# Kernel optimization log

Measured on AMD Instinct MI355X. Metric: run time of the kernel, lower is better.

The kernel has to match this reference:

```python
import jax, jax.numpy as jnp
import numpy as np

B, S, H = 32, 256, 1024   # batch, seq_len, xlmr hidden
HL = 512                  # lstm hidden per direction
E = 256                   # entity_feature_size
L = 5                     # languages: en fr de es it
LN_EPS = 1e-5


def setup_inputs() -> dict:
    key = jax.random.key(0)
    ks = jax.random.split(key, 12)
    sc = 0.02
    sequence_output = jax.random.normal(ks[0], (B, S, H), jnp.float32)
    lengths = jax.random.randint(ks[1], (B,), S // 2, S + 1)
    attention_mask = (jnp.arange(S)[None, :] < lengths[:, None]).astype(jnp.int32)
    language_ids = jax.random.randint(ks[2], (B,), 0, L).astype(jnp.int64)
    # per-language adapter params (stacked over lang dim)
    W1 = jax.random.normal(ks[3], (L, H, H), jnp.float32) * sc
    b1 = jnp.zeros((L, H), jnp.float32)
    ln_g = jnp.ones((L, H), jnp.float32)
    ln_b = jnp.zeros((L, H), jnp.float32)
    W2 = jax.random.normal(ks[4], (L, H, H), jnp.float32) * sc
    b2 = jnp.zeros((L, H), jnp.float32)
    # BiLSTM params, torch gate order (i, f, g, o); b = b_ih + b_hh
    Wih_f = jax.random.normal(ks[5], (4 * HL, H), jnp.float32) * sc
    Whh_f = jax.random.normal(ks[6], (4 * HL, HL), jnp.float32) * sc
    b_f = jnp.zeros((4 * HL,), jnp.float32)
    Wih_b = jax.random.normal(ks[7], (4 * HL, H), jnp.float32) * sc
    Whh_b = jax.random.normal(ks[8], (4 * HL, HL), jnp.float32) * sc
    b_b = jnp.zeros((4 * HL,), jnp.float32)
    # projection 2*HL -> E
    Wp = jax.random.normal(ks[9], (E, 2 * HL), jnp.float32) * sc
    bp = jnp.zeros((E,), jnp.float32)
    return dict(sequence_output=sequence_output, attention_mask=attention_mask,
                language_ids=language_ids, W1=W1, b1=b1, ln_g=ln_g, ln_b=ln_b,
                W2=W2, b2=b2, Wih_f=Wih_f, Whh_f=Whh_f, b_f=b_f,
                Wih_b=Wih_b, Whh_b=Whh_b, b_b=b_b, Wp=Wp, bp=bp)


def _lstm_scan(x, mask, Wih, Whh, b):
    """x: [S,B,H], mask: [S,B,1] bool. Returns hidden states [S,B,HL].
    Masked steps keep state and emit 0 (pack/pad_packed semantics)."""
    h0 = jnp.zeros((x.shape[1], Whh.shape[1]), x.dtype)

    def step(carry, inp):
        h, c = carry
        x_t, m = inp
        gates = x_t @ Wih.T + h @ Whh.T + b
        i, f, g, o = jnp.split(gates, 4, axis=-1)
        c_new = jax.nn.sigmoid(f) * c + jax.nn.sigmoid(i) * jnp.tanh(g)
        h_new = jax.nn.sigmoid(o) * jnp.tanh(c_new)
        h = jnp.where(m, h_new, h)
        c = jnp.where(m, c_new, c)
        return (h, c), jnp.where(m, h_new, 0.0)

    _, ys = jax.lax.scan(step, (h0, h0), (x, mask))
    return ys


def reference(sequence_output, attention_mask, language_ids, W1, b1, ln_g, ln_b,
              W2, b2, Wih_f, Whh_f, b_f, Wih_b, Whh_b, b_b, Wp, bp):
    # --- all 5 language adapters on the full batch, then masked-sum ---
    h = jnp.einsum('bsh,lhd->lbsd', sequence_output, W1) + b1[:, None, None, :]
    mu = h.mean(-1, keepdims=True)
    var = h.var(-1, keepdims=True)
    h = (h - mu) * jax.lax.rsqrt(var + LN_EPS) * ln_g[:, None, None, :] + ln_b[:, None, None, :]
    h = jax.nn.relu(h)
    h = jnp.einsum('lbsd,ldh->lbsh', h, W2) + b2[:, None, None, :]
    onehot = jax.nn.one_hot(language_ids, L, dtype=h.dtype)          # [B,L]
    adapted = jnp.einsum('lbsh,bl->bsh', h, onehot)                  # [B,S,H]
    # --- BiLSTM over valid lengths (packed-sequence semantics) ---
    x = adapted.transpose(1, 0, 2)                                    # [S,B,H]
    m = attention_mask.astype(bool).T[:, :, None]                     # [S,B,1]
    ys_f = _lstm_scan(x, m, Wih_f, Whh_f, b_f)                        # [S,B,HL]
    ys_b = _lstm_scan(x[::-1], m[::-1], Wih_b, Whh_b, b_b)[::-1]      # [S,B,HL]
    lstm_out = jnp.concatenate([ys_f, ys_b], -1).transpose(1, 0, 2)   # [B,S,2HL]
    return lstm_out @ Wp.T + bp                                       # [B,S,E]
```

## Files before the change

kernel.cpp:

```cpp
#include <hip/hip_runtime.h>

typedef __bf16 bft;
typedef bft bf16x8 __attribute__((ext_vector_type(8)));
typedef bft bf16x4 __attribute__((ext_vector_type(4)));
typedef bft bf16x2 __attribute__((ext_vector_type(2)));
typedef float f32x4 __attribute__((ext_vector_type(4)));
typedef unsigned long long u64;
typedef unsigned int u32;
typedef u32 u32x4 __attribute__((ext_vector_type(4)));

#define LN_EPS 1e-5f
#define SENT 0x7FC17FC1u


__device__ __forceinline__ float sigmoidf_(float x) {
    return 1.f / (1.f + __expf(-x));
}
__device__ __forceinline__ float tanhf_(float x) {
    float e = __expf(-2.f * fabsf(x));
    float t = (1.f - e) / (1.f + e);
    return copysignf(t, x);
}

__global__ void cvt_f32_bf16(const float* __restrict__ in, bft* __restrict__ out, int n4) {
    int i = blockIdx.x * blockDim.x + threadIdx.x;
    if (i < n4) {
        float4 v = ((const float4*)in)[i];
        bf16x4 o = { (bft)v.x, (bft)v.y, (bft)v.z, (bft)v.w };
        ((bf16x4*)out)[i] = o;
    }
}

__global__ void init_hg(u32* __restrict__ hg) {
    int i = blockIdx.x * blockDim.x + threadIdx.x;
    int buf = (i >> 13) & 3;
    hg[i] = (buf == 0) ? 0u : SENT;
}

__global__ void pack_mask(const int* __restrict__ mask, u32* __restrict__ mbits) {
    int t = blockIdx.x * blockDim.x + threadIdx.x;
    if (t < 256) {
        int w = t >> 5, b = t & 31;
        u32 v = 0;
        for (int i = 0; i < 32; ++i)
            v |= (mask[b * 256 + w * 32 + i] ? 1u : 0u) << i;
        mbits[w * 32 + b] = v;
    }
}

__global__ __launch_bounds__(256) void cvt_permute_wih(
    const float* __restrict__ in, bft* __restrict__ out)
{
    int r = blockIdx.x;
    int src = (r & 3) * 512 + (r >> 2);
    int t = threadIdx.x;
    float4 v = ((const float4*)(in + (size_t)src * 1024))[t];
    bf16x4 o = { (bft)v.x, (bft)v.y, (bft)v.z, (bft)v.w };
    ((bf16x4*)(out + (size_t)r * 1024))[t] = o;
}

__global__ void permute_bias(const float* __restrict__ in, float* __restrict__ out) {
    int t = blockIdx.x * blockDim.x + threadIdx.x;
    if (t < 2048) out[t] = in[(t & 3) * 512 + (t >> 2)];
}

__global__ __launch_bounds__(256) void transpose_cvt_w(
    const float* __restrict__ W1, const float* __restrict__ W2,
    bft* __restrict__ W1t, bft* __restrict__ W2t)
{
    __shared__ float tile[32][33];
    int z = blockIdx.z;
    int l = z >> 1;
    const float* src = ((z & 1) ? W2 : W1) + ((size_t)l << 20);
    bft* dst = ((z & 1) ? W2t : W1t) + ((size_t)l << 20);
    int tx = threadIdx.x & 31, ty = threadIdx.x >> 5;
    int bx = blockIdx.x * 32, by = blockIdx.y * 32;
    for (int r = ty; r < 32; r += 8)
        tile[r][tx] = src[(size_t)(by + r) * 1024 + bx + tx];
    __syncthreads();
    for (int r = ty; r < 32; r += 8)
        dst[(size_t)(bx + r) * 1024 + by + tx] = (bft)tile[tx][r];
}

__global__ __launch_bounds__(256) void gemm_bt(
    const bft* __restrict__ A, const bft* __restrict__ Bt,
    const float* __restrict__ bias, const int* __restrict__ langs,
    int langStrideB, int langStrideBias,
    float* __restrict__ outF, bft* __restrict__ outB,
    int remapLog, int remapMul, int ldc)
{
    const int K = 1024;
    int tn = blockIdx.x, tm = blockIdx.y;
    int row0 = tm * 128, col0 = tn * 128;
    int lang = langs ? langs[row0 >> 8] : 0;
    const bft* Ap = A + (size_t)row0 * K;
    const bft* Bp = Bt + (size_t)lang * langStrideB + (size_t)col0 * K;
    const float* biasp = bias + (size_t)lang * langStrideBias + col0;

    __shared__ bft As[128 * 32];
    __shared__ bft Bs[128 * 32];

    int t = threadIdx.x;
    int lane = t & 63, wave = t >> 6;
    int wm = wave & 1, wn = wave >> 1;
    int lrow = lane & 15, quad = lane >> 4;

    f32x4 acc[4][4] = {};

    for (int k0 = 0; k0 < K; k0 += 32) {
        __syncthreads();
        for (int c = t; c < 512; c += 256) {
            int r = c >> 2, co = (c & 3) << 3;
            *(uint4*)(As + r * 32 + co) = *(const uint4*)(Ap + (size_t)r * K + k0 + co);
            *(uint4*)(Bs + r * 32 + co) = *(const uint4*)(Bp + (size_t)r * K + k0 + co);
        }
        __syncthreads();
        bf16x8 af[4], bfr[4];
#pragma unroll
        for (int i = 0; i < 4; ++i)
            af[i] = *(const bf16x8*)(As + (wm * 64 + i * 16 + lrow) * 32 + quad * 8);
#pragma unroll
        for (int j = 0; j < 4; ++j)
            bfr[j] = *(const bf16x8*)(Bs + (wn * 64 + j * 16 + lrow) * 32 + quad * 8);
#pragma unroll
        for (int i = 0; i < 4; ++i)
#pragma unroll
            for (int j = 0; j < 4; ++j)
                acc[i][j] = __builtin_amdgcn_mfma_f32_16x16x32_bf16(af[i], bfr[j], acc[i][j], 0, 0, 0);
    }

#pragma unroll
    for (int i = 0; i < 4; ++i) {
#pragma unroll
        for (int j = 0; j < 4; ++j) {
#pragma unroll
            for (int r = 0; r < 4; ++r) {
                int m = wm * 64 + i * 16 + quad * 4 + r;
                int n = wn * 64 + j * 16 + lrow;
                int grow = row0 + m;
                float v = acc[i][j][r] + biasp[n];
                size_t idx;
                if (remapLog < 0) {
                    int b = grow >> 8, s = grow & 255;
                    int col = col0 + n;
                    int jj = col >> 2, gg = col & 3;
                    int jp = jj & 7, gs = jj >> 3;
                    int tc = (((b >> 4) * 2 + (jp >> 2)) << 6) + ((jp & 3) << 4) + (b & 15);
                    idx = (((size_t)s * 64 + gs) << 10) + (tc << 2) + gg;
                } else {
                    int orow = remapLog ? ((grow & ((1 << remapLog) - 1)) * remapMul + (grow >> remapLog))
                                        : grow;
                    idx = (size_t)orow * ldc + col0 + n;
                }
                if (outF) outF[idx] = v;
                else outB[idx] = (bft)v;
            }
        }
    }
}

__global__ __launch_bounds__(256) void ln_relu_kernel(
    const float* __restrict__ h1, bft* __restrict__ a2,
    const float* __restrict__ ln_g, const float* __restrict__ ln_b,
    const int* __restrict__ langs)
{
    int row = blockIdx.x;
    int lang = langs[row >> 8];
    const float* x = h1 + (size_t)row * 1024;
    int t = threadIdx.x;
    float4 v = ((const float4*)x)[t];
    float s = v.x + v.y + v.z + v.w;
    float ss = v.x * v.x + v.y * v.y + v.z * v.z + v.w * v.w;
#pragma unroll
    for (int off = 32; off > 0; off >>= 1) {
        s += __shfl_down(s, off, 64);
        ss += __shfl_down(ss, off, 64);
    }
    __shared__ float red[8];
    int wave = t >> 6, lane = t & 63;
    if (lane == 0) { red[wave] = s; red[4 + wave] = ss; }
    __syncthreads();
    float S = red[0] + red[1] + red[2] + red[3];
    float SS = red[4] + red[5] + red[6] + red[7];
    float mean = S * (1.f / 1024.f);
    float var = SS * (1.f / 1024.f) - mean * mean;
    float inv = rsqrtf(var + LN_EPS);
    float4 g = ((const float4*)(ln_g + (size_t)lang * 1024))[t];
    float4 b = ((const float4*)(ln_b + (size_t)lang * 1024))[t];
    float y0 = fmaxf(0.f, (v.x - mean) * inv * g.x + b.x);
    float y1 = fmaxf(0.f, (v.y - mean) * inv * g.y + b.y);
    float y2 = fmaxf(0.f, (v.z - mean) * inv * g.z + b.z);
    float y3 = fmaxf(0.f, (v.w - mean) * inv * g.w + b.w);
    bf16x4 o = { (bft)y0, (bft)y1, (bft)y2, (bft)y3 };
    ((bf16x4*)(a2 + (size_t)row * 1024))[t] = o;
}

__global__ __launch_bounds__(256) void bilstm_kernel(
    const bft* __restrict__ gin_f, const bft* __restrict__ gin_b,
    const bft* __restrict__ Whh_f, const bft* __restrict__ Whh_b,
    const u32* __restrict__ mbits, bft* __restrict__ ys,
    u32* __restrict__ hg)
{
    __shared__ u64 smem[4096];
    bft* hs  = (bft*)smem;
    u32* hsd = (u32*)smem;

    int blk = blockIdx.x;
    int dir = blk >> 6;
    int gslice = blk & 63;
    const bft* Whh = dir ? Whh_b : Whh_f;
    const bft* gin = dir ? gin_b : gin_f;
    u32* hbase = hg + (size_t)dir * 4 * 8192;

    int t = threadIdx.x;
    int lane = t & 63, wave = t >> 6;
    int wm = wave & 1, wn = wave >> 1;
    int lrow = lane & 15, quad = lane >> 4;

    bf16x8 wf[16];
    {
        int row32 = wm * 16 + lrow;
        int jl = row32 >> 2, g = row32 & 3;
        const bft* wp = Whh + (size_t)(g * 512 + (gslice << 3) + jl) * 512 + quad * 8;
#pragma unroll
        for (int kk = 0; kk < 16; ++kk)
            wf[kk] = *(const bf16x8*)(wp + kk * 32);
    }

    int batch = wn * 16 + lrow;
    u32* ysU = (u32*)ys;
    float cs = 0.f, hp = 0.f;
    u32 mw = 0;

    for (int it = 0; it < 256; ++it) {
        int tt = dir ? (255 - it) : it;

        bf16x4 gv = *(const bf16x4*)(gin + ((((size_t)tt * 64 + gslice) << 10) + (t << 2)));
        if ((it & 31) == 0) mw = mbits[(tt >> 5) * 32 + batch];
        int mk = (mw >> (tt & 31)) & 1;

        if (!(lane & 16)) {
            u32* ca = hbase + (size_t)((it + 2) & 3) * 8192
                            + gslice * 128 + batch * 4 + wm * 2 + (quad >> 1);
            u32 sv = SENT;
            asm volatile("global_store_dword %0, %1, off sc0 sc1" :: "v"(ca), "v"(sv) : "memory");
        }

        __syncthreads();

        const u32* hq = hbase + (size_t)(it & 3) * 8192;
        u32x4 r[8];
        u32 need = 0xffu;
        for (;;) {
#pragma unroll
            for (int i = 0; i < 8; ++i)
                if (need & (1u << i))
                    asm volatile("global_load_dwordx4 %0, %1, off sc0 sc1"
                                 : "=v"(r[i]) : "v"(hq + i * 1024 + t * 4) : "memory");
            asm volatile("s_waitcnt vmcnt(0)" ::: "memory");
#pragma unroll
            for (int i = 0; i < 8; ++i)
                if ((need & (1u << i)) &&
                    r[i][0] != SENT && r[i][1] != SENT && r[i][2] != SENT && r[i][3] != SENT)
                    need &= ~(1u << i);
            if (!need) break;
            __builtin_amdgcn_s_sleep(2);
        }

#pragma unroll
        for (int i = 0; i < 8; ++i) {
            int bat = t & 31, gs = i * 8 + (t >> 5);
            *(u32x4*)(hsd + bat * 256 + ((gs ^ (bat & 7)) << 2)) = r[i];
        }
        __syncthreads();

        f32x4 acc0 = {}, acc1 = {};
#pragma unroll
        for (int kk = 0; kk < 16; ++kk) {
            int b16 = kk * 4 + quad;
            bf16x8 b = *(const bf16x8*)(hs + batch * 512 + ((b16 ^ (batch & 7)) << 3));
            if (kk & 1) acc1 = __builtin_amdgcn_mfma_f32_16x16x32_bf16(wf[kk], b, acc1, 0, 0, 0);
            else        acc0 = __builtin_amdgcn_mfma_f32_16x16x32_bf16(wf[kk], b, acc0, 0, 0, 0);
        }
        f32x4 acc = acc0 + acc1;

        float xi = acc[0] + (float)gv[0];
        float xf = acc[1] + (float)gv[1];
        float xg = acc[2] + (float)gv[2];
        float xo = acc[3] + (float)gv[3];
        float cn = sigmoidf_(xf) * cs + sigmoidf_(xi) * tanhf_(xg);
        float hn = sigmoidf_(xo) * tanhf_(cn);
        if (mk) { cs = cn; hp = hn; }
        union { bft h; unsigned short u; } hc; hc.h = (bft)hp;
        u32 own = (u32)hc.u | ((mk ? (u32)hc.u : 0u) << 16);
        u32 par = __shfl_xor(own, 16, 64);
        u32 hpair = (own & 0xffffu) | (par << 16);
        u32 ypair = (own >> 16) | (par & 0xffff0000u);

        if (!(lane & 16)) {
            u32* ha = hbase + (size_t)((it + 1) & 3) * 8192
                            + gslice * 128 + batch * 4 + wm * 2 + (quad >> 1);
            asm volatile("global_store_dword %0, %1, off sc0 sc1" :: "v"(ha), "v"(hpair) : "memory");
            ysU[((size_t)tt * 32 + batch) * 512 + dir * 256
                + (gslice << 2) + wm * 2 + (quad >> 1)] = ypair;
        }
    }
}

extern "C" void kernel_launch(void* const* d_in, const int* in_sizes, int n_in,
                              void* d_out, int out_size, void* d_ws, size_t ws_size,
                              hipStream_t stream)
{
    const float* X     = (const float*)d_in[0];
    const int*   amask = (const int*)d_in[1];
    const int*   langs = (const int*)d_in[2];
    const float* W1    = (const float*)d_in[3];
    const float* b1    = (const float*)d_in[4];
    const float* ln_g  = (const float*)d_in[5];
    const float* ln_b  = (const float*)d_in[6];
    const float* W2    = (const float*)d_in[7];
    const float* b2    = (const float*)d_in[8];
    const float* Wih_f = (const float*)d_in[9];
    const float* Whh_f = (const float*)d_in[10];
    const float* b_f   = (const float*)d_in[11];
    const float* Wih_b = (const float*)d_in[12];
    const float* Whh_b = (const float*)d_in[13];
    const float* b_b   = (const float*)d_in[14];
    const float* Wp    = (const float*)d_in[15];
    const float* bp    = (const float*)d_in[16];
    float* out = (float*)d_out;

    char* ws = (char*)d_ws;
    size_t off = 0;
    auto alloc = [&](size_t bytes) -> void* {
        void* p = ws + off;
        off += (bytes + 255) & ~(size_t)255;
        return p;
    };
    bft* Xbf   = (bft*)alloc(8192ull * 1024 * 2);
    bft* W1t   = (bft*)alloc(5ull * 1024 * 1024 * 2);
    bft* W2t   = (bft*)alloc(5ull * 1024 * 1024 * 2);
    bft* Wihf  = (bft*)alloc(2048ull * 1024 * 2);
    bft* Wihb  = (bft*)alloc(2048ull * 1024 * 2);
    bft* Whhf  = (bft*)alloc(2048ull * 512 * 2);
    bft* Whhb  = (bft*)alloc(2048ull * 512 * 2);
    bft* Wpb   = (bft*)alloc(256ull * 1024 * 2);
    float* h1  = (float*)alloc(8192ull * 1024 * 4);
    bft* a2    = (bft*)alloc(8192ull * 1024 * 2);
    bft* adapt = (bft*)alloc(8192ull * 1024 * 2);
    bft* ginf  = (bft*)alloc(256ull * 32 * 2048 * 2);
    bft* ginb  = (bft*)alloc(256ull * 32 * 2048 * 2);
    bft* ysb   = (bft*)alloc(256ull * 32 * 1024 * 2);
    float* pbf = (float*)alloc(2048ull * 4);
    float* pbb = (float*)alloc(2048ull * 4);
    u32* hg    = (u32*)alloc(2ull * 4 * 8192 * 4);
    u32* mbits = (u32*)alloc(256ull * 4);
    (void)ws_size; (void)in_sizes; (void)n_in; (void)out_size;

    auto cvt = [&](const float* src, bft* dst, int n) {
        int n4 = n >> 2;
        hipLaunchKernelGGL(cvt_f32_bf16, dim3((n4 + 255) / 256), dim3(256), 0, stream, src, dst, n4);
    };
    cvt(X, Xbf, 8192 * 1024);
    hipLaunchKernelGGL(cvt_permute_wih, dim3(2048), dim3(256), 0, stream, Wih_f, Wihf);
    hipLaunchKernelGGL(cvt_permute_wih, dim3(2048), dim3(256), 0, stream, Wih_b, Wihb);
    cvt(Whh_f, Whhf, 2048 * 512);
    cvt(Whh_b, Whhb, 2048 * 512);
    cvt(Wp, Wpb, 256 * 1024);
    hipLaunchKernelGGL(permute_bias, dim3(8), dim3(256), 0, stream, b_f, pbf);
    hipLaunchKernelGGL(permute_bias, dim3(8), dim3(256), 0, stream, b_b, pbb);
    hipLaunchKernelGGL(init_hg, dim3(256), dim3(256), 0, stream, hg);
    hipLaunchKernelGGL(pack_mask, dim3(1), dim3(256), 0, stream, amask, mbits);
    hipLaunchKernelGGL(transpose_cvt_w, dim3(32, 32, 10), dim3(256), 0, stream, W1, W2, W1t, W2t);

    hipLaunchKernelGGL(gemm_bt, dim3(8, 64), dim3(256), 0, stream,
        Xbf, W1t, b1, langs, 1024 * 1024, 1024, h1, (bft*)nullptr, 0, 0, 1024);
    hipLaunchKernelGGL(ln_relu_kernel, dim3(8192), dim3(256), 0, stream, h1, a2, ln_g, ln_b, langs);
    hipLaunchKernelGGL(gemm_bt, dim3(8, 64), dim3(256), 0, stream,
        a2, W2t, b2, langs, 1024 * 1024, 1024, (float*)nullptr, adapt, 0, 0, 1024);
    hipLaunchKernelGGL(gemm_bt, dim3(16, 64), dim3(256), 0, stream,
        adapt, Wihf, pbf, (const int*)nullptr, 0, 0, (float*)nullptr, ginf, -1, 0, 0);
    hipLaunchKernelGGL(gemm_bt, dim3(16, 64), dim3(256), 0, stream,
        adapt, Wihb, pbb, (const int*)nullptr, 0, 0, (float*)nullptr, ginb, -1, 0, 0);
    {
        void* args[] = { (void*)&ginf, (void*)&ginb, (void*)&Whhf, (void*)&Whhb,
                         (void*)&mbits, (void*)&ysb, (void*)&hg };
        hipLaunchCooperativeKernel((const void*)bilstm_kernel, dim3(128), dim3(256), args, 0, stream);
    }
    hipLaunchKernelGGL(gemm_bt, dim3(2, 64), dim3(256), 0, stream,
        ysb, Wpb, bp, (const int*)nullptr, 0, 0, out, (bft*)nullptr, 5, 256, 256);
}
```

Before: 1.276 ms.

## Load LSTM hidden state directly into MFMA registers and use global_load_lds in GEMM

The BiLSTM recurrence now lays out the global hidden-state exchange buffer batch-major, so each lane loads its MFMA B-operand fragments straight from global memory. This removes the LDS staging and both per-step __syncthreads, and each wave polls for the sentinel independently with a ballot. Block-to-direction mapping is interleaved so both directions spread across the device. The GEMM tile loads switch to global_load_lds to skip the register round trip. In exchange each lane issues twice as many global loads per poll, and the GEMM drops the explicit row/col tile layout, which relies on the linear LDS layout matching.

```diff
diff --git a/kernel.cpp b/kernel.cpp
--- a/kernel.cpp
+++ b/kernel.cpp
@@ -109,10 +109,16 @@
 
     for (int k0 = 0; k0 < K; k0 += 32) {
         __syncthreads();
-        for (int c = t; c < 512; c += 256) {
+#pragma unroll
+        for (int c0 = 0; c0 < 512; c0 += 256) {
+            int c = c0 + t;
             int r = c >> 2, co = (c & 3) << 3;
-            *(uint4*)(As + r * 32 + co) = *(const uint4*)(Ap + (size_t)r * K + k0 + co);
-            *(uint4*)(Bs + r * 32 + co) = *(const uint4*)(Bp + (size_t)r * K + k0 + co);
+            __builtin_amdgcn_global_load_lds(
+                (const __attribute__((address_space(1))) u32*)(Ap + (size_t)r * K + k0 + co),
+                (__attribute__((address_space(3))) u32*)(As + c * 8), 16, 0, 0);
+            __builtin_amdgcn_global_load_lds(
+                (const __attribute__((address_space(1))) u32*)(Bp + (size_t)r * K + k0 + co),
+                (__attribute__((address_space(3))) u32*)(Bs + c * 8), 16, 0, 0);
         }
         __syncthreads();
         bf16x8 af[4], bfr[4];
@@ -201,13 +207,9 @@
     const u32* __restrict__ mbits, bft* __restrict__ ys,
     u32* __restrict__ hg)
 {
-    __shared__ u64 smem[4096];
-    bft* hs  = (bft*)smem;
-    u32* hsd = (u32*)smem;
-
     int blk = blockIdx.x;
-    int dir = blk >> 6;
-    int gslice = blk & 63;
+    int dir = (blk & 7) >> 2;
+    int gslice = ((blk >> 3) << 2) + (blk & 3);
     const bft* Whh = dir ? Whh_b : Whh_f;
     const bft* gin = dir ? gin_b : gin_f;
     u32* hbase = hg + (size_t)dir * 4 * 8192;
@@ -228,6 +230,8 @@
     }
 
     int batch = wn * 16 + lrow;
+    int fbase = batch * 256 + quad * 4;
+    int pword = batch * 256 + (gslice << 2) + wm * 2 + (quad >> 1);
     u32* ysU = (u32*)ys;
     float cs = 0.f, hp = 0.f;
     u32 mw = 0;
@@ -240,47 +244,36 @@
         int mk = (mw >> (tt & 31)) & 1;
 
         if (!(lane & 16)) {
-            u32* ca = hbase + (size_t)((it + 2) & 3) * 8192
-                            + gslice * 128 + batch * 4 + wm * 2 + (quad >> 1);
+            u32* ca = hbase + (size_t)((it + 2) & 3) * 8192 + pword;
             u32 sv = SENT;
             asm volatile("global_store_dword %0, %1, off sc0 sc1" :: "v"(ca), "v"(sv) : "memory");
         }
 
-        __syncthreads();
-
-        const u32* hq = hbase + (size_t)(it & 3) * 8192;
-        u32x4 r[8];
-        u32 need = 0xffu;
+        const u32* hq = hbase + (size_t)(it & 3) * 8192 + fbase;
+        u32x4 r[16];
+        u32 need = 0xffffu;
         for (;;) {
 #pragma unroll
-            for (int i = 0; i < 8; ++i)
+            for (int i = 0; i < 16; ++i)
                 if (need & (1u << i))
                     asm volatile("global_load_dwordx4 %0, %1, off sc0 sc1"
-                                 : "=v"(r[i]) : "v"(hq + i * 1024 + t * 4) : "memory");
+                                 : "=v"(r[i]) : "v"(hq + i * 16) : "memory");
             asm volatile("s_waitcnt vmcnt(0)" ::: "memory");
 #pragma unroll
-            for (int i = 0; i < 8; ++i)
+            for (int i = 0; i < 16; ++i)
                 if ((need & (1u << i)) &&
                     r[i][0] != SENT && r[i][1] != SENT && r[i][2] != SENT && r[i][3] != SENT)
                     need &= ~(1u << i);
-            if (!need) break;
-            __builtin_amdgcn_s_sleep(2);
-        }
-
-#pragma unroll
-        for (int i = 0; i < 8; ++i) {
-            int bat = t & 31, gs = i * 8 + (t >> 5);
-            *(u32x4*)(hsd + bat * 256 + ((gs ^ (bat & 7)) << 2)) = r[i];
-        }
-        __syncthreads();
+            if (!__ballot(need)) break;
+            __builtin_amdgcn_s_sleep(1);
+        }
 
         f32x4 acc0 = {}, acc1 = {};
 #pragma unroll
         for (int kk = 0; kk < 16; ++kk) {
-            int b16 = kk * 4 + quad;
-            bf16x8 b = *(const bf16x8*)(hs + batch * 512 + ((b16 ^ (batch & 7)) << 3));
-            if (kk & 1) acc1 = __builtin_amdgcn_mfma_f32_16x16x32_bf16(wf[kk], b, acc1, 0, 0, 0);
-            else        acc0 = __builtin_amdgcn_mfma_f32_16x16x32_bf16(wf[kk], b, acc0, 0, 0, 0);
+            union { u32x4 u; bf16x8 h; } ub; ub.u = r[kk];
+            if (kk & 1) acc1 = __builtin_amdgcn_mfma_f32_16x16x32_bf16(wf[kk], ub.h, acc1, 0, 0, 0);
+            else        acc0 = __builtin_amdgcn_mfma_f32_16x16x32_bf16(wf[kk], ub.h, acc0, 0, 0, 0);
         }
         f32x4 acc = acc0 + acc1;
 
@@ -298,8 +291,7 @@
         u32 ypair = (own >> 16) | (par & 0xffff0000u);
 
         if (!(lane & 16)) {
-            u32* ha = hbase + (size_t)((it + 1) & 3) * 8192
-                            + gslice * 128 + batch * 4 + wm * 2 + (quad >> 1);
+            u32* ha = hbase + (size_t)((it + 1) & 3) * 8192 + pword;
             asm volatile("global_store_dword %0, %1, off sc0 sc1" :: "v"(ha), "v"(hpair) : "memory");
             ysU[((size_t)tt * 32 + batch) * 512 + dir * 256
                 + (gslice << 2) + wm * 2 + (quad >> 1)] = ypair;
```

Measured after the change: 2.732 ms. 2.14x slower.

## Pin BiLSTM blocks to one XCD, use non-LLC coherence; async LDS loads in GEMM

Applied to the files above, without the earlier changes.

The recurrent kernel now launches 256 blocks and keeps only those whose index mod 8 is 0 or 1. On MI355X this places each direction's 32 blocks on a single XCD, assuming round-robin dispatch. A runtime probe checks that all peer blocks see each other's writes with sc0-only (L2-scope) accesses, and if so runs the step-to-step hidden-state exchange without sc1 system-scope coherence, falling back to the old path otherwise. Each block now handles 16 hidden units and both batch halves, with the gin layout and GEMM epilogue remapped to match. The GEMM tile loads switch to global_load_lds direct-to-LDS transfers. The XCD-placement assumption is hardware-dispatch dependent, and the probe adds a startup handshake.

```diff
diff --git a/kernel.cpp b/kernel.cpp
--- a/kernel.cpp
+++ b/kernel.cpp
@@ -10,7 +10,8 @@
 typedef u32 u32x4 __attribute__((ext_vector_type(4)));
 
 #define LN_EPS 1e-5f
-#define SENT 0x7FC17FC1u
+#define SENT  0x7FC17FC1u
+#define MAGIC 0xA5A5A5A5u
 
 
 __device__ __forceinline__ float sigmoidf_(float x) {
@@ -29,6 +30,11 @@
         bf16x4 o = { (bft)v.x, (bft)v.y, (bft)v.z, (bft)v.w };
         ((bf16x4*)out)[i] = o;
     }
+}
+
+__global__ void zero_u32(u32* __restrict__ p, int n) {
+    int i = blockIdx.x * blockDim.x + threadIdx.x;
+    if (i < n) p[i] = 0u;
 }
 
 __global__ void init_hg(u32* __restrict__ hg) {
@@ -109,10 +115,16 @@
 
     for (int k0 = 0; k0 < K; k0 += 32) {
         __syncthreads();
-        for (int c = t; c < 512; c += 256) {
+#pragma unroll
+        for (int c0 = 0; c0 < 512; c0 += 256) {
+            int c = c0 + t;
             int r = c >> 2, co = (c & 3) << 3;
-            *(uint4*)(As + r * 32 + co) = *(const uint4*)(Ap + (size_t)r * K + k0 + co);
-            *(uint4*)(Bs + r * 32 + co) = *(const uint4*)(Bp + (size_t)r * K + k0 + co);
+            __builtin_amdgcn_global_load_lds(
+                (const __attribute__((address_space(1))) u32*)(Ap + (size_t)r * K + k0 + co),
+                (__attribute__((address_space(3))) u32*)(As + c * 8), 16, 0, 0);
+            __builtin_amdgcn_global_load_lds(
+                (const __attribute__((address_space(1))) u32*)(Bp + (size_t)r * K + k0 + co),
+                (__attribute__((address_space(3))) u32*)(Bs + c * 8), 16, 0, 0);
         }
         __syncthreads();
         bf16x8 af[4], bfr[4];
@@ -144,9 +156,10 @@
                     int b = grow >> 8, s = grow & 255;
                     int col = col0 + n;
                     int jj = col >> 2, gg = col & 3;
-                    int jp = jj & 7, gs = jj >> 3;
-                    int tc = (((b >> 4) * 2 + (jp >> 2)) << 6) + ((jp & 3) << 4) + (b & 15);
-                    idx = (((size_t)s * 64 + gs) << 10) + (tc << 2) + gg;
+                    int gs = jj >> 4, jl = jj & 15;
+                    int ln = (jl >> 2) * 64 + (jl & 3) * 16 + (b & 15);
+                    int e = ((b >> 4) << 2) + gg;
+                    idx = (((size_t)s * 32 + gs) << 11) + ln * 8 + e;
                 } else {
                     int orow = remapLog ? ((grow & ((1 << remapLog) - 1)) * remapMul + (grow >> remapLog))
                                         : grow;
@@ -195,68 +208,65 @@
     ((bf16x4*)(a2 + (size_t)row * 1024))[t] = o;
 }
 
-__global__ __launch_bounds__(256) void bilstm_kernel(
-    const bft* __restrict__ gin_f, const bft* __restrict__ gin_b,
-    const bft* __restrict__ Whh_f, const bft* __restrict__ Whh_b,
-    const u32* __restrict__ mbits, bft* __restrict__ ys,
-    u32* __restrict__ hg)
-{
-    __shared__ u64 smem[4096];
+template<bool LLC>
+__device__ __forceinline__ void st1(u32* p, u32 v) {
+    if constexpr (LLC)
+        asm volatile("global_store_dword %0, %1, off sc0 sc1" :: "v"(p), "v"(v) : "memory");
+    else
+        asm volatile("global_store_dword %0, %1, off sc0" :: "v"(p), "v"(v) : "memory");
+}
+template<bool LLC>
+__device__ __forceinline__ void ld4(u32x4& r, const u32* p) {
+    if constexpr (LLC)
+        asm volatile("global_load_dwordx4 %0, %1, off sc0 sc1" : "=v"(r) : "v"(p) : "memory");
+    else
+        asm volatile("global_load_dwordx4 %0, %1, off sc0" : "=v"(r) : "v"(p) : "memory");
+}
+
+struct Wf { bf16x8 v[16]; };
+
+template<bool LLC>
+__device__ __forceinline__ void lstm_loop(
+    const Wf wf, const bft* __restrict__ gin, const u32* __restrict__ mbits,
+    bft* __restrict__ ys, u32* __restrict__ hbase, u64* smem, int dir, int gslice)
+{
     bft* hs  = (bft*)smem;
     u32* hsd = (u32*)smem;
-
-    int blk = blockIdx.x;
-    int dir = blk >> 6;
-    int gslice = blk & 63;
-    const bft* Whh = dir ? Whh_b : Whh_f;
-    const bft* gin = dir ? gin_b : gin_f;
-    u32* hbase = hg + (size_t)dir * 4 * 8192;
-
     int t = threadIdx.x;
-    int lane = t & 63, wave = t >> 6;
-    int wm = wave & 1, wn = wave >> 1;
+    int lane = t & 63, w = t >> 6;
     int lrow = lane & 15, quad = lane >> 4;
-
-    bf16x8 wf[16];
-    {
-        int row32 = wm * 16 + lrow;
-        int jl = row32 >> 2, g = row32 & 3;
-        const bft* wp = Whh + (size_t)(g * 512 + (gslice << 3) + jl) * 512 + quad * 8;
-#pragma unroll
-        for (int kk = 0; kk < 16; ++kk)
-            wf[kk] = *(const bf16x8*)(wp + kk * 32);
-    }
-
-    int batch = wn * 16 + lrow;
+    int jw = w * 2 + (quad >> 1);
+    int pw0 = gslice * 256 + lrow * 8 + jw;
+    int pw1 = pw0 + 128;
     u32* ysU = (u32*)ys;
-    float cs = 0.f, hp = 0.f;
-    u32 mw = 0;
+    float cs0 = 0.f, cs1 = 0.f, hp0 = 0.f, hp1 = 0.f;
+    u32 mw0 = 0, mw1 = 0;
 
     for (int it = 0; it < 256; ++it) {
         int tt = dir ? (255 - it) : it;
 
-        bf16x4 gv = *(const bf16x4*)(gin + ((((size_t)tt * 64 + gslice) << 10) + (t << 2)));
-        if ((it & 31) == 0) mw = mbits[(tt >> 5) * 32 + batch];
-        int mk = (mw >> (tt & 31)) & 1;
+        bf16x8 gv = *(const bf16x8*)(gin + (((size_t)tt * 32 + gslice) << 11) + t * 8);
+        if ((it & 31) == 0) {
+            mw0 = mbits[(tt >> 5) * 32 + lrow];
+            mw1 = mbits[(tt >> 5) * 32 + 16 + lrow];
+        }
+        int mk0 = (mw0 >> (tt & 31)) & 1;
+        int mk1 = (mw1 >> (tt & 31)) & 1;
 
         if (!(lane & 16)) {
-            u32* ca = hbase + (size_t)((it + 2) & 3) * 8192
-                            + gslice * 128 + batch * 4 + wm * 2 + (quad >> 1);
-            u32 sv = SENT;
-            asm volatile("global_store_dword %0, %1, off sc0 sc1" :: "v"(ca), "v"(sv) : "memory");
-        }
-
-        __syncthreads();
-
-        const u32* hq = hbase + (size_t)(it & 3) * 8192;
+            u32* ca = hbase + (size_t)((it + 2) & 3) * 8192;
+            st1<LLC>(ca + pw0, SENT);
+            st1<LLC>(ca + pw1, SENT);
+        }
+        __syncthreads();
+
+        const u32* hq = hbase + (size_t)(it & 3) * 8192 + t * 4;
         u32x4 r[8];
         u32 need = 0xffu;
         for (;;) {
 #pragma unroll
             for (int i = 0; i < 8; ++i)
-                if (need & (1u << i))
-                    asm volatile("global_load_dwordx4 %0, %1, off sc0 sc1"
-                                 : "=v"(r[i]) : "v"(hq + i * 1024 + t * 4) : "memory");
+                if (need & (1u << i)) ld4<LLC>(r[i], hq + i * 1024);
             asm volatile("s_waitcnt vmcnt(0)" ::: "memory");
 #pragma unroll
             for (int i = 0; i < 8; ++i)
@@ -264,47 +274,142 @@
                     r[i][0] != SENT && r[i][1] != SENT && r[i][2] != SENT && r[i][3] != SENT)
                     need &= ~(1u << i);
             if (!need) break;
-            __builtin_amdgcn_s_sleep(2);
+            __builtin_amdgcn_s_sleep(1);
         }
 
 #pragma unroll
         for (int i = 0; i < 8; ++i) {
-            int bat = t & 31, gs = i * 8 + (t >> 5);
-            *(u32x4*)(hsd + bat * 256 + ((gs ^ (bat & 7)) << 2)) = r[i];
-        }
-        __syncthreads();
-
-        f32x4 acc0 = {}, acc1 = {};
+            int gs  = i * 4 + (t >> 6);
+            int bat = (t & 63) >> 1;
+            int b16 = gs * 2 + (t & 1);
+            *(u32x4*)(hsd + bat * 256 + ((b16 ^ (bat & 7)) << 2)) = r[i];
+        }
+        __syncthreads();
+
+        f32x4 aA = {}, aB = {}, aC = {}, aD = {};
 #pragma unroll
         for (int kk = 0; kk < 16; ++kk) {
             int b16 = kk * 4 + quad;
-            bf16x8 b = *(const bf16x8*)(hs + batch * 512 + ((b16 ^ (batch & 7)) << 3));
-            if (kk & 1) acc1 = __builtin_amdgcn_mfma_f32_16x16x32_bf16(wf[kk], b, acc1, 0, 0, 0);
-            else        acc0 = __builtin_amdgcn_mfma_f32_16x16x32_bf16(wf[kk], b, acc0, 0, 0, 0);
-        }
-        f32x4 acc = acc0 + acc1;
-
-        float xi = acc[0] + (float)gv[0];
-        float xf = acc[1] + (float)gv[1];
-        float xg = acc[2] + (float)gv[2];
-        float xo = acc[3] + (float)gv[3];
-        float cn = sigmoidf_(xf) * cs + sigmoidf_(xi) * tanhf_(xg);
-        float hn = sigmoidf_(xo) * tanhf_(cn);
-        if (mk) { cs = cn; hp = hn; }
-        union { bft h; unsigned short u; } hc; hc.h = (bft)hp;
-        u32 own = (u32)hc.u | ((mk ? (u32)hc.u : 0u) << 16);
-        u32 par = __shfl_xor(own, 16, 64);
-        u32 hpair = (own & 0xffffu) | (par << 16);
-        u32 ypair = (own >> 16) | (par & 0xffff0000u);
+            int bat1 = 16 + lrow;
+            bf16x8 b0 = *(const bf16x8*)(hs + lrow * 512 + ((b16 ^ (lrow & 7)) << 3));
+            bf16x8 b1 = *(const bf16x8*)(hs + bat1 * 512 + ((b16 ^ (bat1 & 7)) << 3));
+            if (kk & 1) {
+                aB = __builtin_amdgcn_mfma_f32_16x16x32_bf16(wf.v[kk], b0, aB, 0, 0, 0);
+                aD = __builtin_amdgcn_mfma_f32_16x16x32_bf16(wf.v[kk], b1, aD, 0, 0, 0);
+            } else {
+                aA = __builtin_amdgcn_mfma_f32_16x16x32_bf16(wf.v[kk], b0, aA, 0, 0, 0);
+                aC = __builtin_amdgcn_mfma_f32_16x16x32_bf16(wf.v[kk], b1, aC, 0, 0, 0);
+            }
+        }
+        f32x4 a0 = aA + aB, a1 = aC + aD;
+
+        float xi0 = a0[0] + (float)gv[0], xf0 = a0[1] + (float)gv[1];
+        float xg0 = a0[2] + (float)gv[2], xo0 = a0[3] + (float)gv[3];
+        float xi1 = a1[0] + (float)gv[4], xf1 = a1[1] + (float)gv[5];
+        float xg1 = a1[2] + (float)gv[6], xo1 = a1[3] + (float)gv[7];
+        float cn0 = sigmoidf_(xf0) * cs0 + sigmoidf_(xi0) * tanhf_(xg0);
+        float cn1 = sigmoidf_(xf1) * cs1 + sigmoidf_(xi1) * tanhf_(xg1);
+        float hn0 = sigmoidf_(xo0) * tanhf_(cn0);
+        float hn1 = sigmoidf_(xo1) * tanhf_(cn1);
+        if (mk0) { cs0 = cn0; hp0 = hn0; }
+        if (mk1) { cs1 = cn1; hp1 = hn1; }
+        union { bft h; unsigned short u; } h0c, h1c;
+        h0c.h = (bft)hp0; h1c.h = (bft)hp1;
+        u32 own0 = (u32)h0c.u | ((mk0 ? (u32)h0c.u : 0u) << 16);
+        u32 own1 = (u32)h1c.u | ((mk1 ? (u32)h1c.u : 0u) << 16);
+        u32 par0 = __shfl_xor(own0, 16, 64);
+        u32 par1 = __shfl_xor(own1, 16, 64);
 
         if (!(lane & 16)) {
-            u32* ha = hbase + (size_t)((it + 1) & 3) * 8192
-                            + gslice * 128 + batch * 4 + wm * 2 + (quad >> 1);
-            asm volatile("global_store_dword %0, %1, off sc0 sc1" :: "v"(ha), "v"(hpair) : "memory");
-            ysU[((size_t)tt * 32 + batch) * 512 + dir * 256
-                + (gslice << 2) + wm * 2 + (quad >> 1)] = ypair;
-        }
-    }
+            u32 hw0 = (own0 & 0xffffu) | (par0 << 16);
+            u32 hw1 = (own1 & 0xffffu) | (par1 << 16);
+            u32 yw0 = (own0 >> 16) | (par0 & 0xffff0000u);
+            u32 yw1 = (own1 >> 16) | (par1 & 0xffff0000u);
+            u32* ha = hbase + (size_t)((it + 1) & 3) * 8192;
+            st1<LLC>(ha + pw0, hw0);
+            st1<LLC>(ha + pw1, hw1);
+            ysU[((size_t)tt * 32 + lrow) * 512 + dir * 256 + gslice * 8 + jw] = yw0;
+            ysU[((size_t)tt * 32 + 16 + lrow) * 512 + dir * 256 + gslice * 8 + jw] = yw1;
+        }
+    }
+}
+
+__global__ __launch_bounds__(256) void bilstm_kernel(
+    const bft* __restrict__ gin_f, const bft* __restrict__ gin_b,
+    const bft* __restrict__ Whh_f, const bft* __restrict__ Whh_b,
+    const u32* __restrict__ mbits, bft* __restrict__ ys,
+    u32* __restrict__ hg, u32* __restrict__ probe)
+{
+    int blk = blockIdx.x;
+    if ((blk & 7) > 1) return;
+    int dir = blk & 7;
+    int gslice = blk >> 3;
+    const bft* Whh = dir ? Whh_b : Whh_f;
+    const bft* gin = dir ? gin_b : gin_f;
+    u32* hbase = hg + (size_t)dir * 4 * 8192;
+
+    __shared__ u64 smem[4096];
+    u32* hsd = (u32*)smem;
+
+    int t = threadIdx.x;
+    int lane = t & 63, w = t >> 6;
+    int lrow = lane & 15, quad = lane >> 4;
+
+    Wf wf;
+    {
+        int jl = w * 4 + (lrow >> 2), g = lrow & 3;
+        const bft* wp = Whh + (size_t)(g * 512 + gslice * 16 + jl) * 512 + quad * 8;
+#pragma unroll
+        for (int kk = 0; kk < 16; ++kk)
+            wf.v[kk] = *(const bf16x8*)(wp + kk * 32);
+    }
+
+    u32* pr = probe + dir * 32;
+    u32* vd = probe + 64 + dir * 32;
+    if (t == 0) {
+        u32 m = MAGIC;
+        asm volatile("global_store_dword %0, %1, off sc0" :: "v"(pr + gslice), "v"(m) : "memory");
+    }
+    int fast;
+    {
+        int ok = 0;
+        if (w == 0) {
+            const u32* pp = pr + (lane & 31);
+            for (int rd = 0; rd < 96; ++rd) {
+                u32 v;
+                asm volatile("global_load_dword %0, %1, off sc0" : "=v"(v) : "v"(pp) : "memory");
+                asm volatile("s_waitcnt vmcnt(0)" ::: "memory");
+                if (__all(v == MAGIC)) { ok = 1; break; }
+                __builtin_amdgcn_s_sleep(4);
+            }
+        }
+        if (t == 0) hsd[0] = (u32)ok;
+        __syncthreads();
+        ok = (int)hsd[0];
+        __syncthreads();
+        if (t == 0) {
+            u32 v = ok ? 1u : 2u;
+            asm volatile("global_store_dword %0, %1, off sc0 sc1" :: "v"(vd + gslice), "v"(v) : "memory");
+        }
+        int f2 = 0;
+        if (w == 0) {
+            const u32* pp = vd + (lane & 31);
+            for (;;) {
+                u32 v;
+                asm volatile("global_load_dword %0, %1, off sc0 sc1" : "=v"(v) : "v"(pp) : "memory");
+                asm volatile("s_waitcnt vmcnt(0)" ::: "memory");
+                if (__all(v != 0u)) { f2 = __all(v == 1u) ? 1 : 0; break; }
+                __builtin_amdgcn_s_sleep(4);
+            }
+        }
+        if (t == 0) hsd[0] = (u32)f2;
+        __syncthreads();
+        fast = (int)hsd[0];
+        __syncthreads();
+    }
+
+    if (fast) lstm_loop<false>(wf, gin, mbits, ys, hbase, smem, dir, gslice);
+    else      lstm_loop<true >(wf, gin, mbits, ys, hbase, smem, dir, gslice);
 }
 
 extern "C" void kernel_launch(void* const* d_in, const int* in_sizes, int n_in,
@@ -355,6 +460,7 @@
     float* pbb = (float*)alloc(2048ull * 4);
     u32* hg    = (u32*)alloc(2ull * 4 * 8192 * 4);
     u32* mbits = (u32*)alloc(256ull * 4);
+    u32* probe = (u32*)alloc(128ull * 4);
     (void)ws_size; (void)in_sizes; (void)n_in; (void)out_size;
 
     auto cvt = [&](const float* src, bft* dst, int n) {
@@ -370,6 +476,7 @@
     hipLaunchKernelGGL(permute_bias, dim3(8), dim3(256), 0, stream, b_f, pbf);
     hipLaunchKernelGGL(permute_bias, dim3(8), dim3(256), 0, stream, b_b, pbb);
     hipLaunchKernelGGL(init_hg, dim3(256), dim3(256), 0, stream, hg);
+    hipLaunchKernelGGL(zero_u32, dim3(1), dim3(256), 0, stream, probe, 128);
     hipLaunchKernelGGL(pack_mask, dim3(1), dim3(256), 0, stream, amask, mbits);
     hipLaunchKernelGGL(transpose_cvt_w, dim3(32, 32, 10), dim3(256), 0, stream, W1, W2, W1t, W2t);
 
@@ -384,8 +491,8 @@
         adapt, Wihb, pbb, (const int*)nullptr, 0, 0, (float*)nullptr, ginb, -1, 0, 0);
     {
         void* args[] = { (void*)&ginf, (void*)&ginb, (void*)&Whhf, (void*)&Whhb,
-                         (void*)&mbits, (void*)&ysb, (void*)&hg };
-        hipLaunchCooperativeKernel((const void*)bilstm_kernel, dim3(128), dim3(256), args, 0, stream);
+                         (void*)&mbits, (void*)&ysb, (void*)&hg, (void*)&probe };
+        hipLaunchCooperativeKernel((const void*)bilstm_kernel, dim3(256), dim3(256), args, 0, stream);
     }
     hipLaunchKernelGGL(gemm_bt, dim3(2, 64), dim3(256), 0, stream,
         ysb, Wpb, bp, (const int*)nullptr, 0, 0, out, (bft*)nullptr, 5, 256, 256);
```

Result: slower. 1.693 ms (+32.7%).

## Interleave forward and backward LSTM directions in one block, use direct LDS loads in GEMM

Applied to the files above, without the earlier changes.

The BiLSTM kernel now runs both directions in each of 64 blocks instead of one direction per block across 128 blocks. Each step alternates forward polling and compute with backward polling and compute, so one direction's global-memory barrier latency can overlap the other's work. The GEMM staging loop now uses global_load_lds to copy tiles straight into shared memory without going through registers, and the poll sleep is shortened. The cost is double the register weight fragments per thread, fewer blocks in flight, and each block doing twice the serial work per step.

```diff
diff --git a/kernel.cpp b/kernel.cpp
--- a/kernel.cpp
+++ b/kernel.cpp
@@ -109,10 +109,16 @@
 
     for (int k0 = 0; k0 < K; k0 += 32) {
         __syncthreads();
-        for (int c = t; c < 512; c += 256) {
+#pragma unroll
+        for (int c0 = 0; c0 < 512; c0 += 256) {
+            int c = c0 + t;
             int r = c >> 2, co = (c & 3) << 3;
-            *(uint4*)(As + r * 32 + co) = *(const uint4*)(Ap + (size_t)r * K + k0 + co);
-            *(uint4*)(Bs + r * 32 + co) = *(const uint4*)(Bp + (size_t)r * K + k0 + co);
+            __builtin_amdgcn_global_load_lds(
+                (const __attribute__((address_space(1))) u32*)(Ap + (size_t)r * K + k0 + co),
+                (__attribute__((address_space(3))) u32*)(As + c * 8), 16, 0, 0);
+            __builtin_amdgcn_global_load_lds(
+                (const __attribute__((address_space(1))) u32*)(Bp + (size_t)r * K + k0 + co),
+                (__attribute__((address_space(3))) u32*)(Bs + c * 8), 16, 0, 0);
         }
         __syncthreads();
         bf16x8 af[4], bfr[4];
@@ -195,114 +201,141 @@
     ((bf16x4*)(a2 + (size_t)row * 1024))[t] = o;
 }
 
-__global__ __launch_bounds__(256) void bilstm_kernel(
+__device__ __forceinline__ void poll_stage(const u32* __restrict__ hq0,
+                                           u32* __restrict__ hsd, int t)
+{
+    const u32* hq = hq0 + t * 4;
+    u32x4 r[8];
+    u32 need = 0xffu;
+    for (;;) {
+#pragma unroll
+        for (int i = 0; i < 8; ++i)
+            if (need & (1u << i))
+                asm volatile("global_load_dwordx4 %0, %1, off sc0 sc1"
+                             : "=v"(r[i]) : "v"(hq + i * 1024) : "memory");
+        asm volatile("s_waitcnt vmcnt(0)" ::: "memory");
+#pragma unroll
+        for (int i = 0; i < 8; ++i)
+            if ((need & (1u << i)) &&
+                r[i][0] != SENT && r[i][1] != SENT && r[i][2] != SENT && r[i][3] != SENT)
+                need &= ~(1u << i);
+        if (!need) break;
+        __builtin_amdgcn_s_sleep(1);
+    }
+#pragma unroll
+    for (int i = 0; i < 8; ++i) {
+        int bat = t & 31, gs = i * 8 + (t >> 5);
+        *(u32x4*)(hsd + bat * 256 + ((gs ^ (bat & 7)) << 2)) = r[i];
+    }
+}
+
+__device__ __forceinline__ void step_phase(
+    const bf16x8* __restrict__ wf, const bft* __restrict__ hs,
+    int batch, int quad, bf16x4 gv, int mk,
+    float& cs, float& hp, u32& hpair, u32& ypair)
+{
+    f32x4 acc0 = {}, acc1 = {};
+#pragma unroll
+    for (int kk = 0; kk < 16; ++kk) {
+        int b16 = kk * 4 + quad;
+        bf16x8 b = *(const bf16x8*)(hs + batch * 512 + ((b16 ^ (batch & 7)) << 3));
+        if (kk & 1) acc1 = __builtin_amdgcn_mfma_f32_16x16x32_bf16(wf[kk], b, acc1, 0, 0, 0);
+        else        acc0 = __builtin_amdgcn_mfma_f32_16x16x32_bf16(wf[kk], b, acc0, 0, 0, 0);
+    }
+    f32x4 acc = acc0 + acc1;
+    float xi = acc[0] + (float)gv[0];
+    float xf = acc[1] + (float)gv[1];
+    float xg = acc[2] + (float)gv[2];
+    float xo = acc[3] + (float)gv[3];
+    float cn = sigmoidf_(xf) * cs + sigmoidf_(xi) * tanhf_(xg);
+    float hn = sigmoidf_(xo) * tanhf_(cn);
+    if (mk) { cs = cn; hp = hn; }
+    union { bft h; unsigned short u; } hc; hc.h = (bft)hp;
+    u32 own = (u32)hc.u | ((mk ? (u32)hc.u : 0u) << 16);
+    u32 par = __shfl_xor(own, 16, 64);
+    hpair = (own & 0xffffu) | (par << 16);
+    ypair = (own >> 16) | (par & 0xffff0000u);
+}
+
+__global__ __launch_bounds__(256, 1) void bilstm_kernel(
     const bft* __restrict__ gin_f, const bft* __restrict__ gin_b,
     const bft* __restrict__ Whh_f, const bft* __restrict__ Whh_b,
     const u32* __restrict__ mbits, bft* __restrict__ ys,
     u32* __restrict__ hg)
 {
-    __shared__ u64 smem[4096];
-    bft* hs  = (bft*)smem;
-    u32* hsd = (u32*)smem;
-
-    int blk = blockIdx.x;
-    int dir = blk >> 6;
-    int gslice = blk & 63;
-    const bft* Whh = dir ? Whh_b : Whh_f;
-    const bft* gin = dir ? gin_b : gin_f;
-    u32* hbase = hg + (size_t)dir * 4 * 8192;
+    __shared__ u64 smem[8192];
+    bft* hsf  = (bft*)smem;
+    u32* hsfd = (u32*)smem;
+    bft* hsb  = (bft*)(smem + 4096);
+    u32* hsbd = (u32*)(smem + 4096);
+
+    int gslice = blockIdx.x;
+    int jbase = gslice << 3;
+    u32* hbf = hg;
+    u32* hbb = hg + 4 * 8192;
 
     int t = threadIdx.x;
     int lane = t & 63, wave = t >> 6;
     int wm = wave & 1, wn = wave >> 1;
     int lrow = lane & 15, quad = lane >> 4;
 
-    bf16x8 wf[16];
+    bf16x8 wff[16], wfb[16];
     {
         int row32 = wm * 16 + lrow;
         int jl = row32 >> 2, g = row32 & 3;
-        const bft* wp = Whh + (size_t)(g * 512 + (gslice << 3) + jl) * 512 + quad * 8;
-#pragma unroll
-        for (int kk = 0; kk < 16; ++kk)
-            wf[kk] = *(const bf16x8*)(wp + kk * 32);
+        const bft* wpf = Whh_f + (size_t)(g * 512 + jbase + jl) * 512 + quad * 8;
+        const bft* wpb = Whh_b + (size_t)(g * 512 + jbase + jl) * 512 + quad * 8;
+#pragma unroll
+        for (int kk = 0; kk < 16; ++kk) {
+            wff[kk] = *(const bf16x8*)(wpf + kk * 32);
+            wfb[kk] = *(const bf16x8*)(wpb + kk * 32);
+        }
     }
 
     int batch = wn * 16 + lrow;
+    int pword = gslice * 128 + batch * 4 + wm * 2 + (quad >> 1);
     u32* ysU = (u32*)ys;
-    float cs = 0.f, hp = 0.f;
-    u32 mw = 0;
+    float csf = 0.f, hpf = 0.f, csb = 0.f, hpb = 0.f;
+    u32 mwf = 0, mwb = 0;
 
     for (int it = 0; it < 256; ++it) {
-        int tt = dir ? (255 - it) : it;
-
-        bf16x4 gv = *(const bf16x4*)(gin + ((((size_t)tt * 64 + gslice) << 10) + (t << 2)));
-        if ((it & 31) == 0) mw = mbits[(tt >> 5) * 32 + batch];
-        int mk = (mw >> (tt & 31)) & 1;
+        int ttf = it, ttb = 255 - it;
+
+        bf16x4 gvf = *(const bf16x4*)(gin_f + ((((size_t)ttf * 64 + gslice) << 10) + (t << 2)));
+        bf16x4 gvb = *(const bf16x4*)(gin_b + ((((size_t)ttb * 64 + gslice) << 10) + (t << 2)));
+        if ((it & 31) == 0) {
+            mwf = mbits[(ttf >> 5) * 32 + batch];
+            mwb = mbits[(ttb >> 5) * 32 + batch];
+        }
+        int mkf = (mwf >> (ttf & 31)) & 1;
+        int mkb = (mwb >> (ttb & 31)) & 1;
 
         if (!(lane & 16)) {
-            u32* ca = hbase + (size_t)((it + 2) & 3) * 8192
-                            + gslice * 128 + batch * 4 + wm * 2 + (quad >> 1);
             u32 sv = SENT;
-            asm volatile("global_store_dword %0, %1, off sc0 sc1" :: "v"(ca), "v"(sv) : "memory");
-        }
-
+            u32* caf = hbf + (size_t)((it + 2) & 3) * 8192 + pword;
+            u32* cab = hbb + (size_t)((it + 2) & 3) * 8192 + pword;
+            asm volatile("global_store_dword %0, %1, off sc0 sc1" :: "v"(caf), "v"(sv) : "memory");
+            asm volatile("global_store_dword %0, %1, off sc0 sc1" :: "v"(cab), "v"(sv) : "memory");
+        }
+
+        poll_stage(hbf + (size_t)(it & 3) * 8192, hsfd, t);
         __syncthreads();
-
-        const u32* hq = hbase + (size_t)(it & 3) * 8192;
-        u32x4 r[8];
-        u32 need = 0xffu;
-        for (;;) {
-#pragma unroll
-            for (int i = 0; i < 8; ++i)
-                if (need & (1u << i))
-                    asm volatile("global_load_dwordx4 %0, %1, off sc0 sc1"
-                                 : "=v"(r[i]) : "v"(hq + i * 1024 + t * 4) : "memory");
-            asm volatile("s_waitcnt vmcnt(0)" ::: "memory");
-#pragma unroll
-            for (int i = 0; i < 8; ++i)
-                if ((need & (1u << i)) &&
-                    r[i][0] != SENT && r[i][1] != SENT && r[i][2] != SENT && r[i][3] != SENT)
-                    need &= ~(1u << i);
-            if (!need) break;
-            __builtin_amdgcn_s_sleep(2);
-        }
-
-#pragma unroll
-        for (int i = 0; i < 8; ++i) {
-            int bat = t & 31, gs = i * 8 + (t >> 5);
-            *(u32x4*)(hsd + bat * 256 + ((gs ^ (bat & 7)) << 2)) = r[i];
-        }
+        u32 hwf, ywf;
+        step_phase(wff, hsf, batch, quad, gvf, mkf, csf, hpf, hwf, ywf);
+        if (!(lane & 16)) {
+            u32* ha = hbf + (size_t)((it + 1) & 3) * 8192 + pword;
+            asm volatile("global_store_dword %0, %1, off sc0 sc1" :: "v"(ha), "v"(hwf) : "memory");
+            ysU[((size_t)ttf * 32 + batch) * 512 + (gslice << 2) + wm * 2 + (quad >> 1)] = ywf;
+        }
+
+        poll_stage(hbb + (size_t)(it & 3) * 8192, hsbd, t);
         __syncthreads();
-
-        f32x4 acc0 = {}, acc1 = {};
-#pragma unroll
-        for (int kk = 0; kk < 16; ++kk) {
-            int b16 = kk * 4 + quad;
-            bf16x8 b = *(const bf16x8*)(hs + batch * 512 + ((b16 ^ (batch & 7)) << 3));
-            if (kk & 1) acc1 = __builtin_amdgcn_mfma_f32_16x16x32_bf16(wf[kk], b, acc1, 0, 0, 0);
-            else        acc0 = __builtin_amdgcn_mfma_f32_16x16x32_bf16(wf[kk], b, acc0, 0, 0, 0);
-        }
-        f32x4 acc = acc0 + acc1;
-
-        float xi = acc[0] + (float)gv[0];
-        float xf = acc[1] + (float)gv[1];
-        float xg = acc[2] + (float)gv[2];
-        float xo = acc[3] + (float)gv[3];
-        float cn = sigmoidf_(xf) * cs + sigmoidf_(xi) * tanhf_(xg);
-        float hn = sigmoidf_(xo) * tanhf_(cn);
-        if (mk) { cs = cn; hp = hn; }
-        union { bft h; unsigned short u; } hc; hc.h = (bft)hp;
-        u32 own = (u32)hc.u | ((mk ? (u32)hc.u : 0u) << 16);
-        u32 par = __shfl_xor(own, 16, 64);
-        u32 hpair = (own & 0xffffu) | (par << 16);
-        u32 ypair = (own >> 16) | (par & 0xffff0000u);
-
+        u32 hwb, ywb;
+        step_phase(wfb, hsb, batch, quad, gvb, mkb, csb, hpb, hwb, ywb);
         if (!(lane & 16)) {
-            u32* ha = hbase + (size_t)((it + 1) & 3) * 8192
-                            + gslice * 128 + batch * 4 + wm * 2 + (quad >> 1);
-            asm volatile("global_store_dword %0, %1, off sc0 sc1" :: "v"(ha), "v"(hpair) : "memory");
-            ysU[((size_t)tt * 32 + batch) * 512 + dir * 256
-                + (gslice << 2) + wm * 2 + (quad >> 1)] = ypair;
+            u32* ha = hbb + (size_t)((it + 1) & 3) * 8192 + pword;
+            asm volatile("global_store_dword %0, %1, off sc0 sc1" :: "v"(ha), "v"(hwb) : "memory");
+            ysU[((size_t)ttb * 32 + batch) * 512 + 256 + (gslice << 2) + wm * 2 + (quad >> 1)] = ywb;
         }
     }
 }
@@ -385,7 +418,7 @@
     {
         void* args[] = { (void*)&ginf, (void*)&ginb, (void*)&Whhf, (void*)&Whhb,
                          (void*)&mbits, (void*)&ysb, (void*)&hg };
-        hipLaunchCooperativeKernel((const void*)bilstm_kernel, dim3(128), dim3(256), args, 0, stream);
+        hipLaunchCooperativeKernel((const void*)bilstm_kernel, dim3(64), dim3(256), args, 0, stream);
     }
     hipLaunchKernelGGL(gemm_bt, dim3(2, 64), dim3(256), 0, stream,
         ysb, Wpb, bp, (const int*)nullptr, 0, 0, out, (bft*)nullptr, 5, 256, 256);
```

Result: slower. 1.510 ms (+18.4%).
